# Kernel tuning notes

Hardware: AMD Instinct MI355X
Metric: run time of the kernel (lower is better)

## Reference

```python
import jax, jax.numpy as jnp
import numpy as np

N_NODES = 50000
N_EDGES = 800000
IN_DIM, HID_DIM, OUT_DIM = 128, 128, 64


def setup_inputs() -> dict:
    key = jax.random.key(0)
    ks = jax.random.split(key, 8)
    x = jax.random.normal(ks[0], (N_NODES, IN_DIM), dtype=jnp.float32)
    edge_index = jax.random.randint(ks[1], (2, N_EDGES), 0, N_NODES, dtype=jnp.int64)
    # GCNConv uses Glorot weights + zero bias; any random init is fine for a reference
    W1 = jax.random.normal(ks[2], (IN_DIM, HID_DIM), dtype=jnp.float32) / np.sqrt(IN_DIM)
    b1 = jnp.zeros((HID_DIM,), dtype=jnp.float32)
    W2 = jax.random.normal(ks[3], (HID_DIM, OUT_DIM), dtype=jnp.float32) / np.sqrt(HID_DIM)
    b2 = jnp.zeros((OUT_DIM,), dtype=jnp.float32)
    Wfc = jax.random.normal(ks[4], (OUT_DIM, 2), dtype=jnp.float32) / np.sqrt(OUT_DIM)
    bfc = jnp.zeros((2,), dtype=jnp.float32)
    return {"x": x, "edge_index": edge_index, "W1": W1, "b1": b1,
            "W2": W2, "b2": b2, "Wfc": Wfc, "bfc": bfc}


def _gcn_conv(x, src, dst, W, b, n_nodes):
    """PyG GCNConv: out = D^{-1/2} (A+I) D^{-1/2} (x W) + b."""
    xw = x @ W  # [N, F_out] transform before propagation
    ones = jnp.ones(src.shape[0], dtype=xw.dtype)
    deg = jax.ops.segment_sum(ones, dst, num_segments=n_nodes) + 1.0  # +1 for self-loop
    dinv = jax.lax.rsqrt(deg)
    norm = dinv[src] * dinv[dst]  # [E]
    msg = xw[src] * norm[:, None]  # gather + scale: [E, F_out]
    agg = jax.ops.segment_sum(msg, dst, num_segments=n_nodes)  # scatter-add
    agg = agg + xw * (dinv * dinv)[:, None]  # self-loop contribution (norm = 1/deg)
    return agg + b


def reference(x, edge_index, W1, b1, W2, b2, Wfc, bfc):
    n = x.shape[0]
    src, dst = edge_index[0], edge_index[1]
    h = jax.nn.relu(_gcn_conv(x, src, dst, W1, b1, n))
    # dropout is identity in eval mode
    h = _gcn_conv(h, src, dst, W2, b2, n)
    h = h @ Wfc + bfc
    return jax.nn.leaky_relu(h, negative_slope=0.01)
```

## Files before the change

### kernel.cpp

```cpp
#include <hip/hip_runtime.h>
#include <hip/hip_fp16.h>

#define IN_DIM 128
#define HID_DIM 128
#define OUT_DIM 64
#define BINW 128
#define BINSHIFT 7
#define MAXBIN 512
#define EBLK 256

__global__ __launch_bounds__(256) void k_bin_hist(const int* __restrict__ dst,
                                                  int* __restrict__ hist, int E, int nbin) {
    __shared__ int h[MAXBIN];
    int tid = threadIdx.x;
    for (int k = tid; k < nbin; k += 256) h[k] = 0;
    __syncthreads();
    int per = E / gridDim.x;
    int base = blockIdx.x * per;
    int end = (blockIdx.x + 1 == gridDim.x) ? E : base + per;
    for (int i = base + tid; i < end; i += 256)
        atomicAdd(&h[dst[i] >> BINSHIFT], 1);
    __syncthreads();
    for (int k = tid; k < nbin; k += 256) hist[k * EBLK + blockIdx.x] = h[k];
}

__global__ __launch_bounds__(256) void k_bin_scan(int* __restrict__ hist,
                                                  int* __restrict__ total) {
    __shared__ int part[256];
    int k = blockIdx.x;
    int t = threadIdx.x;
    int v = hist[k * EBLK + t];
    part[t] = v;
    __syncthreads();
    for (int off = 1; off < 256; off <<= 1) {
        int u = (t >= off) ? part[t - off] : 0;
        __syncthreads();
        part[t] += u;
        __syncthreads();
    }
    hist[k * EBLK + t] = part[t] - v;
    if (t == 255) total[k] = part[255];
}

__global__ __launch_bounds__(256) void k_bin_base(const int* __restrict__ total,
                                                  int* __restrict__ bin_base, int nbin) {
    __shared__ int part[256];
    int t = threadIdx.x;
    int carry = 0;
    for (int base = 0; base < nbin; base += 256) {
        int i = base + t;
        int v = (i < nbin) ? total[i] : 0;
        part[t] = v;
        __syncthreads();
        for (int off = 1; off < 256; off <<= 1) {
            int u = (t >= off) ? part[t - off] : 0;
            __syncthreads();
            part[t] += u;
            __syncthreads();
        }
        if (i < nbin) bin_base[i] = carry + part[t] - v;
        carry += part[255];
        __syncthreads();
    }
    if (t == 0) bin_base[nbin] = carry;
}

__global__ __launch_bounds__(256) void k_bin_scatter(const int* __restrict__ src,
                                                     const int* __restrict__ dst,
                                                     const int* __restrict__ hist,
                                                     const int* __restrict__ bin_base,
                                                     unsigned int* __restrict__ ebin,
                                                     int E, int nbin) {
    __shared__ int off[MAXBIN];
    int tid = threadIdx.x;
    for (int k = tid; k < nbin; k += 256)
        off[k] = bin_base[k] + hist[k * EBLK + blockIdx.x];
    __syncthreads();
    int per = E / gridDim.x;
    int base = blockIdx.x * per;
    int end = (blockIdx.x + 1 == gridDim.x) ? E : base + per;
    for (int i = base + tid; i < end; i += 256) {
        unsigned int s = (unsigned int)src[i];
        unsigned int d = (unsigned int)dst[i];
        int pos = atomicAdd(&off[d >> BINSHIFT], 1);
        ebin[pos] = s | (d << 16);
    }
}

__global__ __launch_bounds__(256) void k_bin_fill(const unsigned int* __restrict__ ebin,
                                                  const int* __restrict__ bin_base,
                                                  int* __restrict__ row_ptr,
                                                  int* __restrict__ csr_src,
                                                  float* __restrict__ dinv, int N, int nbin) {
    __shared__ int cnt[BINW];
    __shared__ int excl[BINW];
    __shared__ int start[BINW];
    int k = blockIdx.x;
    int node0 = k * BINW;
    int nn = min(BINW, N - node0);
    int t = threadIdx.x;
    if (t < BINW) cnt[t] = 0;
    __syncthreads();
    int eb = bin_base[k], ee = bin_base[k + 1];
    for (int i = eb + t; i < ee; i += 256)
        atomicAdd(&cnt[(ebin[i] >> 16) - node0], 1);
    __syncthreads();
    if (t < BINW) excl[t] = (t < nn) ? cnt[t] : 0;
    __syncthreads();
    for (int off = 1; off < BINW; off <<= 1) {
        int u = 0;
        if (t < BINW && t >= off) u = excl[t - off];
        __syncthreads();
        if (t < BINW) excl[t] += u;
        __syncthreads();
    }
    if (t < nn) {
        int deg = cnt[t];
        int e0 = eb + excl[t] - deg;
        start[t] = e0;
        row_ptr[node0 + t] = e0;
        dinv[node0 + t] = rsqrtf((float)deg + 1.0f);
        cnt[t] = 0;
    }
    if (k == nbin - 1 && t == 0) row_ptr[N] = ee;
    __syncthreads();
    for (int i = eb + t; i < ee; i += 256) {
        unsigned int e = ebin[i];
        int s = (int)(e & 0xffffu);
        int dl = (int)(e >> 16) - node0;
        int slot = start[dl] + atomicAdd(&cnt[dl], 1);
        csr_src[slot] = s;
    }
}

__global__ __launch_bounds__(256) void k_wc(const float* __restrict__ W2,
                                            const float* __restrict__ Wfc,
                                            const float* __restrict__ b2,
                                            const float* __restrict__ bfc,
                                            float* __restrict__ Wc,
                                            float* __restrict__ bc) {
    int t = threadIdx.x;
    int k = t >> 1, j = t & 1;
    float acc = 0.f;
#pragma unroll 8
    for (int m = 0; m < OUT_DIM; ++m) acc += W2[k * OUT_DIM + m] * Wfc[m * 2 + j];
    Wc[k * 2 + j] = acc;
    if (k == 0) {
        float b = 0.f;
#pragma unroll 8
        for (int m = 0; m < OUT_DIM; ++m) b += b2[m] * Wfc[m * 2 + j];
        bc[j] = b + bfc[j];
    }
}

__global__ __launch_bounds__(256) void k_gemm1(const float* __restrict__ x,
                                               const float* __restrict__ W,
                                               const float* __restrict__ dinv,
                                               __half* __restrict__ xwh, int N) {
    __shared__ float Ws[128][128];
    int tid = threadIdx.x;
    const float4* W4 = (const float4*)W;
    float4* Ws4 = (float4*)&Ws[0][0];
#pragma unroll
    for (int i = 0; i < 16; ++i) Ws4[tid + 256 * i] = W4[tid + 256 * i];
    __syncthreads();
    int tx = tid & 15, ty = tid >> 4;
    int row0 = blockIdx.x * 128;
    int rows[8];
    const float* xr[8];
#pragma unroll
    for (int j = 0; j < 8; ++j) {
        int row = row0 + ty + 16 * j;
        rows[j] = row;
        if (row > N - 1) row = N - 1;
        xr[j] = x + (size_t)row * IN_DIM;
    }
    float4 aclo[8], achi[8];
#pragma unroll
    for (int j = 0; j < 8; ++j) {
        aclo[j] = make_float4(0.f, 0.f, 0.f, 0.f);
        achi[j] = make_float4(0.f, 0.f, 0.f, 0.f);
    }
#pragma unroll 2
    for (int k4 = 0; k4 < 32; ++k4) {
        float4 av[8];
#pragma unroll
        for (int j = 0; j < 8; ++j) av[j] = *(const float4*)(xr[j] + k4 * 4);
#pragma unroll
        for (int kk = 0; kk < 4; ++kk) {
            float4 blo = *(const float4*)&Ws[k4 * 4 + kk][4 * tx];
            float4 bhi = *(const float4*)&Ws[k4 * 4 + kk][64 + 4 * tx];
#pragma unroll
            for (int j = 0; j < 8; ++j) {
                float a = (kk == 0) ? av[j].x : (kk == 1) ? av[j].y : (kk == 2) ? av[j].z : av[j].w;
                aclo[j].x += a * blo.x; aclo[j].y += a * blo.y;
                aclo[j].z += a * blo.z; aclo[j].w += a * blo.w;
                achi[j].x += a * bhi.x; achi[j].y += a * bhi.y;
                achi[j].z += a * bhi.z; achi[j].w += a * bhi.w;
            }
        }
    }
#pragma unroll
    for (int j = 0; j < 8; ++j) {
        if (rows[j] < N) {
            float dd = dinv[rows[j]];
            union { __half2 h[2]; uint2 u; } lo, hi;
            lo.h[0] = __floats2half2_rn(aclo[j].x * dd, aclo[j].y * dd);
            lo.h[1] = __floats2half2_rn(aclo[j].z * dd, aclo[j].w * dd);
            hi.h[0] = __floats2half2_rn(achi[j].x * dd, achi[j].y * dd);
            hi.h[1] = __floats2half2_rn(achi[j].z * dd, achi[j].w * dd);
            uint2* p = (uint2*)(xwh + (size_t)rows[j] * HID_DIM);
            p[tx] = lo.u;
            p[16 + tx] = hi.u;
        }
    }
}

__global__ __launch_bounds__(256) void k_agg1z(const int* __restrict__ row_ptr,
                                               const int* __restrict__ csr_src,
                                               const float* __restrict__ dinv,
                                               const __half* __restrict__ xwh,
                                               const float* __restrict__ b1,
                                               const float* __restrict__ Wc,
                                               float* __restrict__ z, int N) {
    constexpr int F = HID_DIM;
    constexpr int L = F / 8;
    constexpr int EPW = 64 / L;
    __shared__ float Wcs[HID_DIM * 2];
    int tid = threadIdx.x;
    if (tid < 64) ((float4*)Wcs)[tid] = ((const float4*)Wc)[tid];
    __syncthreads();
    int node = (blockIdx.x * 256 + tid) >> 6;
    if (node >= N) return;
    int lane = tid & 63;
    int sub = lane / L;
    int c   = lane % L;
    int beg = row_ptr[node], end = row_ptr[node + 1];
    float dd = dinv[node];
    uint4 us = *(const uint4*)(xwh + (size_t)node * F + c * 8);
    float4 b1a = *(const float4*)(b1 + c * 8);
    float4 b1b = *(const float4*)(b1 + c * 8 + 4);
    float a0 = 0.f, a1 = 0.f, a2 = 0.f, a3 = 0.f;
    float a4 = 0.f, a5 = 0.f, a6 = 0.f, a7 = 0.f;
    int j = beg + sub;
    for (; j + EPW < end; j += 2 * EPW) {
        int s0 = csr_src[j];
        int s1 = csr_src[j + EPW];
        uint4 u0 = *(const uint4*)(xwh + (size_t)s0 * F + c * 8);
        uint4 u1 = *(const uint4*)(xwh + (size_t)s1 * F + c * 8);
        float2 v0 = __half22float2(*(__half2*)&u0.x);
        float2 v1 = __half22float2(*(__half2*)&u0.y);
        float2 v2 = __half22float2(*(__half2*)&u0.z);
        float2 v3 = __half22float2(*(__half2*)&u0.w);
        a0 += v0.x; a1 += v0.y; a2 += v1.x; a3 += v1.y;
        a4 += v2.x; a5 += v2.y; a6 += v3.x; a7 += v3.y;
        v0 = __half22float2(*(__half2*)&u1.x);
        v1 = __half22float2(*(__half2*)&u1.y);
        v2 = __half22float2(*(__half2*)&u1.z);
        v3 = __half22float2(*(__half2*)&u1.w);
        a0 += v0.x; a1 += v0.y; a2 += v1.x; a3 += v1.y;
        a4 += v2.x; a5 += v2.y; a6 += v3.x; a7 += v3.y;
    }
    if (j < end) {
        int s = csr_src[j];
        uint4 u = *(const uint4*)(xwh + (size_t)s * F + c * 8);
        float2 v0 = __half22float2(*(__half2*)&u.x);
        float2 v1 = __half22float2(*(__half2*)&u.y);
        float2 v2 = __half22float2(*(__half2*)&u.z);
        float2 v3 = __half22float2(*(__half2*)&u.w);
        a0 += v0.x; a1 += v0.y; a2 += v1.x; a3 += v1.y;
        a4 += v2.x; a5 += v2.y; a6 += v3.x; a7 += v3.y;
    }
#pragma unroll
    for (int off = L; off < 64; off <<= 1) {
        a0 += __shfl_xor(a0, off); a1 += __shfl_xor(a1, off);
        a2 += __shfl_xor(a2, off); a3 += __shfl_xor(a3, off);
        a4 += __shfl_xor(a4, off); a5 += __shfl_xor(a5, off);
        a6 += __shfl_xor(a6, off); a7 += __shfl_xor(a7, off);
    }
    float2 v0 = __half22float2(*(__half2*)&us.x);
    float2 v1 = __half22float2(*(__half2*)&us.y);
    float2 v2 = __half22float2(*(__half2*)&us.z);
    float2 v3 = __half22float2(*(__half2*)&us.w);
    float h[8];
    h[0] = fmaxf((a0 + v0.x) * dd + b1a.x, 0.f);
    h[1] = fmaxf((a1 + v0.y) * dd + b1a.y, 0.f);
    h[2] = fmaxf((a2 + v1.x) * dd + b1a.z, 0.f);
    h[3] = fmaxf((a3 + v1.y) * dd + b1a.w, 0.f);
    h[4] = fmaxf((a4 + v2.x) * dd + b1b.x, 0.f);
    h[5] = fmaxf((a5 + v2.y) * dd + b1b.y, 0.f);
    h[6] = fmaxf((a6 + v3.x) * dd + b1b.z, 0.f);
    h[7] = fmaxf((a7 + v3.y) * dd + b1b.w, 0.f);
    float o0 = 0.f, o1 = 0.f;
#pragma unroll
    for (int k = 0; k < 8; ++k) {
        o0 += h[k] * Wcs[(c * 8 + k) * 2 + 0];
        o1 += h[k] * Wcs[(c * 8 + k) * 2 + 1];
    }
#pragma unroll
    for (int off = 1; off < L; off <<= 1) {
        o0 += __shfl_xor(o0, off);
        o1 += __shfl_xor(o1, off);
    }
    if (lane == 0) {
        float2 r; r.x = o0 * dd; r.y = o1 * dd;
        *(float2*)(z + (size_t)node * 2) = r;
    }
}

__global__ __launch_bounds__(256) void k_agg2(const int* __restrict__ row_ptr,
                                              const int* __restrict__ csr_src,
                                              const float* __restrict__ dinv,
                                              const float* __restrict__ z,
                                              const float* __restrict__ bc,
                                              float* __restrict__ out, int N) {
    int tid = threadIdx.x;
    int gwave = (blockIdx.x * 256 + tid) >> 6;
    int lane = tid & 63;
    int grp = lane >> 3, li = lane & 7;
    int node = gwave * 8 + grp;
    if (node >= N) return;
    int beg = row_ptr[node], end = row_ptr[node + 1];
    float s0 = 0.f, s1 = 0.f;
    int j = beg + li;
    for (; j + 8 < end; j += 16) {
        int sa = csr_src[j];
        int sb = csr_src[j + 8];
        float2 za = *(const float2*)(z + (size_t)sa * 2);
        float2 zb = *(const float2*)(z + (size_t)sb * 2);
        s0 += za.x + zb.x; s1 += za.y + zb.y;
    }
    if (j < end) {
        int s = csr_src[j];
        float2 zv = *(const float2*)(z + (size_t)s * 2);
        s0 += zv.x; s1 += zv.y;
    }
#pragma unroll
    for (int off = 1; off < 8; off <<= 1) {
        s0 += __shfl_xor(s0, off);
        s1 += __shfl_xor(s1, off);
    }
    if (li == 0) {
        float2 zs = *(const float2*)(z + (size_t)node * 2);
        float dd = dinv[node];
        float o0 = (s0 + zs.x) * dd + bc[0];
        float o1 = (s1 + zs.y) * dd + bc[1];
        float2 r;
        r.x = o0 > 0.f ? o0 : 0.01f * o0;
        r.y = o1 > 0.f ? o1 : 0.01f * o1;
        *(float2*)(out + (size_t)node * 2) = r;
    }
}

extern "C" void kernel_launch(void* const* d_in, const int* in_sizes, int n_in,
                              void* d_out, int out_size, void* d_ws, size_t ws_size,
                              hipStream_t stream) {
    const float* x   = (const float*)d_in[0];
    const int*   ei  = (const int*)d_in[1];
    const float* W1  = (const float*)d_in[2];
    const float* b1  = (const float*)d_in[3];
    const float* W2  = (const float*)d_in[4];
    const float* b2  = (const float*)d_in[5];
    const float* Wfc = (const float*)d_in[6];
    const float* bfc = (const float*)d_in[7];

    const int N = in_sizes[0] / IN_DIM;
    const int E = in_sizes[1] / 2;
    const int* src = ei;
    const int* dst = ei + E;
    const int nbin = (N + BINW - 1) / BINW;

    char* base = (char*)d_ws;
    size_t off = 0;
    auto take = [&](size_t bytes) { size_t o = off; off = (off + bytes + 255) & ~(size_t)255; return (void*)(base + o); };
    int*    row_ptr  = (int*)take((size_t)(N + 1) * 4);
    int*    csr_src  = (int*)take((size_t)E * 4);
    int*    hist     = (int*)take((size_t)nbin * EBLK * 4);
    int*    total    = (int*)take((size_t)nbin * 4);
    int*    bin_base = (int*)take((size_t)(nbin + 1) * 4);
    unsigned int* ebin = (unsigned int*)take((size_t)E * 4);
    float*  dinv     = (float*)take((size_t)N * 4);
    __half* xw1h     = (__half*)take((size_t)N * HID_DIM * 2);
    float*  zbuf     = (float*)take((size_t)N * 2 * 4);
    float*  Wc       = (float*)take((size_t)HID_DIM * 2 * 4);
    float*  bc       = (float*)take(2 * 4);

    k_bin_hist<<<EBLK, 256, 0, stream>>>(dst, hist, E, nbin);
    k_bin_scan<<<nbin, 256, 0, stream>>>(hist, total);
    k_bin_base<<<1, 256, 0, stream>>>(total, bin_base, nbin);
    k_bin_scatter<<<EBLK, 256, 0, stream>>>(src, dst, hist, bin_base, ebin, E, nbin);
    k_bin_fill<<<nbin, 256, 0, stream>>>(ebin, bin_base, row_ptr, csr_src, dinv, N, nbin);

    k_wc<<<1, 256, 0, stream>>>(W2, Wfc, b2, bfc, Wc, bc);

    const int nTile = (N + 127) / 128;

    k_gemm1<<<nTile, 256, 0, stream>>>(x, W1, dinv, xw1h, N);
    k_agg1z<<<(N + 3) / 4, 256, 0, stream>>>(row_ptr, csr_src, dinv, xw1h, b1, Wc, zbuf, N);
    const int nAgg2 = ((N + 7) / 8 * 64 + 255) / 256;
    k_agg2<<<nAgg2, 256, 0, stream>>>(row_ptr, csr_src, dinv, zbuf, bc, (float*)d_out, N);
}
```

Measured before the change: 180.3 us.

## Fuse CSR build kernels into one cooperative kernel and shrink csr_src to 16-bit

Replaces the five CSR-construction kernels and the Wc fold kernel with a single cooperative launch of nbin blocks that uses grid-wide syncs between histogram, scan, base, scatter and fill phases. The edge partition now uses nbin blocks instead of 256, so the per-bin scan runs over nblk entries with a wider stride. The CSR source array is also stored as unsigned short, which halves the index traffic in both aggregation kernels. The aim is to remove several launch gaps; the cost is grid.sync overhead and a 16-bit index that only holds for N up to 65536.

```diff
diff --git a/kernel.cpp b/kernel.cpp
--- a/kernel.cpp
+++ b/kernel.cpp
@@ -1,5 +1,8 @@
 #include <hip/hip_runtime.h>
 #include <hip/hip_fp16.h>
+#include <hip/hip_cooperative_groups.h>
+
+namespace cg = cooperative_groups;
 
 #define IN_DIM 128
 #define HID_DIM 128
@@ -7,149 +10,146 @@
 #define BINW 128
 #define BINSHIFT 7
 #define MAXBIN 512
-#define EBLK 256
-
-__global__ __launch_bounds__(256) void k_bin_hist(const int* __restrict__ dst,
-                                                  int* __restrict__ hist, int E, int nbin) {
+#define HSTRIDE 400
+
+__global__ __launch_bounds__(256) void k_build(const int* __restrict__ src,
+                                               const int* __restrict__ dst,
+                                               int* __restrict__ hist,
+                                               int* __restrict__ total,
+                                               int* __restrict__ bin_base,
+                                               unsigned int* __restrict__ ebin,
+                                               int* __restrict__ row_ptr,
+                                               unsigned short* __restrict__ csr_src,
+                                               float* __restrict__ dinv,
+                                               const float* __restrict__ W2,
+                                               const float* __restrict__ Wfc,
+                                               const float* __restrict__ b2,
+                                               const float* __restrict__ bfc,
+                                               float* __restrict__ Wc,
+                                               float* __restrict__ bc,
+                                               int E, int N, int nbin) {
+    cg::grid_group grid = cg::this_grid();
     __shared__ int h[MAXBIN];
-    int tid = threadIdx.x;
-    for (int k = tid; k < nbin; k += 256) h[k] = 0;
-    __syncthreads();
-    int per = E / gridDim.x;
-    int base = blockIdx.x * per;
-    int end = (blockIdx.x + 1 == gridDim.x) ? E : base + per;
-    for (int i = base + tid; i < end; i += 256)
-        atomicAdd(&h[dst[i] >> BINSHIFT], 1);
-    __syncthreads();
-    for (int k = tid; k < nbin; k += 256) hist[k * EBLK + blockIdx.x] = h[k];
-}
-
-__global__ __launch_bounds__(256) void k_bin_scan(int* __restrict__ hist,
-                                                  int* __restrict__ total) {
     __shared__ int part[256];
-    int k = blockIdx.x;
-    int t = threadIdx.x;
-    int v = hist[k * EBLK + t];
-    part[t] = v;
-    __syncthreads();
-    for (int off = 1; off < 256; off <<= 1) {
-        int u = (t >= off) ? part[t - off] : 0;
-        __syncthreads();
-        part[t] += u;
-        __syncthreads();
-    }
-    hist[k * EBLK + t] = part[t] - v;
-    if (t == 255) total[k] = part[255];
-}
-
-__global__ __launch_bounds__(256) void k_bin_base(const int* __restrict__ total,
-                                                  int* __restrict__ bin_base, int nbin) {
-    __shared__ int part[256];
-    int t = threadIdx.x;
-    int carry = 0;
-    for (int base = 0; base < nbin; base += 256) {
-        int i = base + t;
-        int v = (i < nbin) ? total[i] : 0;
-        part[t] = v;
-        __syncthreads();
-        for (int off = 1; off < 256; off <<= 1) {
-            int u = (t >= off) ? part[t - off] : 0;
-            __syncthreads();
-            part[t] += u;
-            __syncthreads();
-        }
-        if (i < nbin) bin_base[i] = carry + part[t] - v;
-        carry += part[255];
-        __syncthreads();
-    }
-    if (t == 0) bin_base[nbin] = carry;
-}
-
-__global__ __launch_bounds__(256) void k_bin_scatter(const int* __restrict__ src,
-                                                     const int* __restrict__ dst,
-                                                     const int* __restrict__ hist,
-                                                     const int* __restrict__ bin_base,
-                                                     unsigned int* __restrict__ ebin,
-                                                     int E, int nbin) {
-    __shared__ int off[MAXBIN];
-    int tid = threadIdx.x;
-    for (int k = tid; k < nbin; k += 256)
-        off[k] = bin_base[k] + hist[k * EBLK + blockIdx.x];
-    __syncthreads();
-    int per = E / gridDim.x;
-    int base = blockIdx.x * per;
-    int end = (blockIdx.x + 1 == gridDim.x) ? E : base + per;
-    for (int i = base + tid; i < end; i += 256) {
-        unsigned int s = (unsigned int)src[i];
-        unsigned int d = (unsigned int)dst[i];
-        int pos = atomicAdd(&off[d >> BINSHIFT], 1);
-        ebin[pos] = s | (d << 16);
-    }
-}
-
-__global__ __launch_bounds__(256) void k_bin_fill(const unsigned int* __restrict__ ebin,
-                                                  const int* __restrict__ bin_base,
-                                                  int* __restrict__ row_ptr,
-                                                  int* __restrict__ csr_src,
-                                                  float* __restrict__ dinv, int N, int nbin) {
     __shared__ int cnt[BINW];
     __shared__ int excl[BINW];
     __shared__ int start[BINW];
-    int k = blockIdx.x;
-    int node0 = k * BINW;
-    int nn = min(BINW, N - node0);
     int t = threadIdx.x;
-    if (t < BINW) cnt[t] = 0;
+    int blk = blockIdx.x;
+    int nblk = gridDim.x;
+    int per = E / nblk;
+    int ebeg = blk * per;
+    int eend = (blk + 1 == nblk) ? E : ebeg + per;
+
+    for (int k = t; k < nbin; k += 256) h[k] = 0;
     __syncthreads();
-    int eb = bin_base[k], ee = bin_base[k + 1];
-    for (int i = eb + t; i < ee; i += 256)
-        atomicAdd(&cnt[(ebin[i] >> 16) - node0], 1);
+    for (int i = ebeg + t; i < eend; i += 256)
+        atomicAdd(&h[dst[i] >> BINSHIFT], 1);
     __syncthreads();
-    if (t < BINW) excl[t] = (t < nn) ? cnt[t] : 0;
+    for (int k = t; k < nbin; k += 256) hist[k * HSTRIDE + blk] = h[k];
+    grid.sync();
+
+    {
+        int k = blk;
+        int carry = 0;
+        for (int base = 0; base < nblk; base += 256) {
+            int i = base + t;
+            int v = (i < nblk) ? hist[k * HSTRIDE + i] : 0;
+            part[t] = v;
+            __syncthreads();
+            for (int off = 1; off < 256; off <<= 1) {
+                int u = (t >= off) ? part[t - off] : 0;
+                __syncthreads();
+                part[t] += u;
+                __syncthreads();
+            }
+            if (i < nblk) hist[k * HSTRIDE + i] = carry + part[t] - v;
+            carry += part[255];
+            __syncthreads();
+        }
+        if (t == 0) total[k] = carry;
+    }
+    grid.sync();
+
+    if (blk == 0) {
+        int carry = 0;
+        for (int base = 0; base < nbin; base += 256) {
+            int i = base + t;
+            int v = (i < nbin) ? total[i] : 0;
+            part[t] = v;
+            __syncthreads();
+            for (int off = 1; off < 256; off <<= 1) {
+                int u = (t >= off) ? part[t - off] : 0;
+                __syncthreads();
+                part[t] += u;
+                __syncthreads();
+            }
+            if (i < nbin) bin_base[i] = carry + part[t] - v;
+            carry += part[255];
+            __syncthreads();
+        }
+        if (t == 0) bin_base[nbin] = carry;
+    } else if (blk == 1) {
+        int k = t >> 1, j = t & 1;
+        float acc = 0.f;
+#pragma unroll 8
+        for (int m = 0; m < OUT_DIM; ++m) acc += W2[k * OUT_DIM + m] * Wfc[m * 2 + j];
+        Wc[k * 2 + j] = acc;
+        if (k == 0) {
+            float b = 0.f;
+#pragma unroll 8
+            for (int m = 0; m < OUT_DIM; ++m) b += b2[m] * Wfc[m * 2 + j];
+            bc[j] = b + bfc[j];
+        }
+    }
+    grid.sync();
+
+    for (int k = t; k < nbin; k += 256)
+        h[k] = bin_base[k] + hist[k * HSTRIDE + blk];
     __syncthreads();
-    for (int off = 1; off < BINW; off <<= 1) {
-        int u = 0;
-        if (t < BINW && t >= off) u = excl[t - off];
+    for (int i = ebeg + t; i < eend; i += 256) {
+        unsigned int s = (unsigned int)src[i];
+        unsigned int d = (unsigned int)dst[i];
+        int pos = atomicAdd(&h[d >> BINSHIFT], 1);
+        ebin[pos] = s | (d << 16);
+    }
+    grid.sync();
+
+    {
+        int k = blk;
+        int node0 = k * BINW;
+        int nn = min(BINW, N - node0);
+        if (t < BINW) cnt[t] = 0;
         __syncthreads();
-        if (t < BINW) excl[t] += u;
+        int eb = bin_base[k], ee = bin_base[k + 1];
+        for (int i = eb + t; i < ee; i += 256)
+            atomicAdd(&cnt[(ebin[i] >> 16) - node0], 1);
         __syncthreads();
-    }
-    if (t < nn) {
-        int deg = cnt[t];
-        int e0 = eb + excl[t] - deg;
-        start[t] = e0;
-        row_ptr[node0 + t] = e0;
-        dinv[node0 + t] = rsqrtf((float)deg + 1.0f);
-        cnt[t] = 0;
-    }
-    if (k == nbin - 1 && t == 0) row_ptr[N] = ee;
-    __syncthreads();
-    for (int i = eb + t; i < ee; i += 256) {
-        unsigned int e = ebin[i];
-        int s = (int)(e & 0xffffu);
-        int dl = (int)(e >> 16) - node0;
-        int slot = start[dl] + atomicAdd(&cnt[dl], 1);
-        csr_src[slot] = s;
-    }
-}
-
-__global__ __launch_bounds__(256) void k_wc(const float* __restrict__ W2,
-                                            const float* __restrict__ Wfc,
-                                            const float* __restrict__ b2,
-                                            const float* __restrict__ bfc,
-                                            float* __restrict__ Wc,
-                                            float* __restrict__ bc) {
-    int t = threadIdx.x;
-    int k = t >> 1, j = t & 1;
-    float acc = 0.f;
-#pragma unroll 8
-    for (int m = 0; m < OUT_DIM; ++m) acc += W2[k * OUT_DIM + m] * Wfc[m * 2 + j];
-    Wc[k * 2 + j] = acc;
-    if (k == 0) {
-        float b = 0.f;
-#pragma unroll 8
-        for (int m = 0; m < OUT_DIM; ++m) b += b2[m] * Wfc[m * 2 + j];
-        bc[j] = b + bfc[j];
+        if (t < BINW) excl[t] = (t < nn) ? cnt[t] : 0;
+        __syncthreads();
+        for (int off = 1; off < BINW; off <<= 1) {
+            int u = 0;
+            if (t < BINW && t >= off) u = excl[t - off];
+            __syncthreads();
+            if (t < BINW) excl[t] += u;
+            __syncthreads();
+        }
+        if (t < nn) {
+            int deg = cnt[t];
+            int e0 = eb + excl[t] - deg;
+            start[t] = e0;
+            row_ptr[node0 + t] = e0;
+            dinv[node0 + t] = rsqrtf((float)deg + 1.0f);
+            cnt[t] = 0;
+        }
+        if (k == nbin - 1 && t == 0) row_ptr[N] = ee;
+        __syncthreads();
+        for (int i = eb + t; i < ee; i += 256) {
+            unsigned int e = ebin[i];
+            int dl = (int)(e >> 16) - node0;
+            int slot = start[dl] + atomicAdd(&cnt[dl], 1);
+            csr_src[slot] = (unsigned short)(e & 0xffffu);
+        }
     }
 }
 
@@ -217,7 +217,7 @@
 }
 
 __global__ __launch_bounds__(256) void k_agg1z(const int* __restrict__ row_ptr,
-                                               const int* __restrict__ csr_src,
+                                               const unsigned short* __restrict__ csr_src,
                                                const float* __restrict__ dinv,
                                                const __half* __restrict__ xwh,
                                                const float* __restrict__ b1,
@@ -309,7 +309,7 @@
 }
 
 __global__ __launch_bounds__(256) void k_agg2(const int* __restrict__ row_ptr,
-                                              const int* __restrict__ csr_src,
+                                              const unsigned short* __restrict__ csr_src,
                                               const float* __restrict__ dinv,
                                               const float* __restrict__ z,
                                               const float* __restrict__ bc,
@@ -374,8 +374,8 @@
     size_t off = 0;
     auto take = [&](size_t bytes) { size_t o = off; off = (off + bytes + 255) & ~(size_t)255; return (void*)(base + o); };
     int*    row_ptr  = (int*)take((size_t)(N + 1) * 4);
-    int*    csr_src  = (int*)take((size_t)E * 4);
-    int*    hist     = (int*)take((size_t)nbin * EBLK * 4);
+    unsigned short* csr_src = (unsigned short*)take((size_t)E * 2);
+    int*    hist     = (int*)take((size_t)nbin * HSTRIDE * 4);
     int*    total    = (int*)take((size_t)nbin * 4);
     int*    bin_base = (int*)take((size_t)(nbin + 1) * 4);
     unsigned int* ebin = (unsigned int*)take((size_t)E * 4);
@@ -385,13 +385,17 @@
     float*  Wc       = (float*)take((size_t)HID_DIM * 2 * 4);
     float*  bc       = (float*)take(2 * 4);
 
-    k_bin_hist<<<EBLK, 256, 0, stream>>>(dst, hist, E, nbin);
-    k_bin_scan<<<nbin, 256, 0, stream>>>(hist, total);
-    k_bin_base<<<1, 256, 0, stream>>>(total, bin_base, nbin);
-    k_bin_scatter<<<EBLK, 256, 0, stream>>>(src, dst, hist, bin_base, ebin, E, nbin);
-    k_bin_fill<<<nbin, 256, 0, stream>>>(ebin, bin_base, row_ptr, csr_src, dinv, N, nbin);
-
-    k_wc<<<1, 256, 0, stream>>>(W2, Wfc, b2, bfc, Wc, bc);
+    {
+        int E_ = E, N_ = N, nbin_ = nbin;
+        void* args[] = {(void*)&src, (void*)&dst, (void*)&hist, (void*)&total,
+                        (void*)&bin_base, (void*)&ebin, (void*)&row_ptr,
+                        (void*)&csr_src, (void*)&dinv,
+                        (void*)&W2, (void*)&Wfc, (void*)&b2, (void*)&bfc,
+                        (void*)&Wc, (void*)&bc,
+                        (void*)&E_, (void*)&N_, (void*)&nbin_};
+        hipLaunchCooperativeKernel((void*)k_build, dim3(nbin), dim3(256),
+                                   args, 0, stream);
+    }
 
     const int nTile = (N + 127) / 128;
 
```

New measurement: 380.7 us. 111% more time.
